# Kernel tuning notes

Hardware: AMD Instinct MI355X
Metric: run time of the kernel (lower is better)

## Reference

```python
import jax, jax.numpy as jnp
import numpy as np

NUM_ENT, NUM_REL, ES = 100000, 200, 128
B, N, K = 4, 1024, 50  # batch of tasks, triples per task, max one-hop neighbors


def setup_inputs() -> dict:
    key = jax.random.key(0)
    ks = jax.random.split(key, 10)
    return {
        "ent_emb": jax.random.normal(ks[0], (NUM_ENT, ES), jnp.float32),
        "rel_emb": jax.random.normal(ks[1], (NUM_REL, ES), jnp.float32),
        "W_bil": jax.random.normal(ks[2], (ES, ES), jnp.float32) * 0.05,
        "W1": jax.random.normal(ks[3], (ES, ES), jnp.float32) * 0.05,
        "b1": jax.random.normal(ks[4], (ES,), jnp.float32) * 0.05,
        "W2": jax.random.normal(ks[5], (ES, ES), jnp.float32) * 0.05,
        "b2": jax.random.normal(ks[6], (ES,), jnp.float32) * 0.05,
        "head_idx": jax.random.randint(ks[7], (B, N), 0, NUM_ENT, jnp.int64),
        "tail_idx": jax.random.randint(ks[8], (B, N), 0, NUM_ENT, jnp.int64),
        "conn_rel": jax.random.randint(ks[9], (NUM_ENT, K), 0, NUM_REL, jnp.int64),
    }


def reference(ent_emb, rel_emb, W_bil, W1, b1, W2, b2, head_idx, tail_idx, conn_rel):
    # Gather head/tail entity embeddings: [B, N, es]
    h_e = ent_emb[head_idx]
    t_e = ent_emb[tail_idx]
    weak_rel = t_e - h_e  # weak relation signal, [B, N, es]

    # Gather one-hop relation embeddings of head/tail neighborhoods: [B, N, K, es]
    h_rel = rel_emb[conn_rel[head_idx]]
    t_rel = rel_emb[conn_rel[tail_idx]]

    # Bilinear score (out_features=1, no bias): score = x1 @ W @ x2
    ws = jnp.einsum('ij,bnj->bni', W_bil, weak_rel)       # [B, N, es]
    h_att = jax.nn.softmax(jnp.einsum('bnki,bni->bnk', h_rel, ws), axis=-1)
    t_att = jax.nn.softmax(jnp.einsum('bnki,bni->bnk', t_rel, ws), axis=-1)

    # Attention-weighted aggregate over neighbors: [B, N, es]
    head = jnp.einsum('bnk,bnki->bni', h_att, h_rel)
    tail = jnp.einsum('bnk,bnki->bni', t_att, t_rel)

    # Fused linear + relu (torch Linear: x @ W.T + b)
    h = jax.nn.relu(head @ W1.T + b1 + h_e @ W2.T + b2)
    t = jax.nn.relu(tail @ W1.T + b1 + t_e @ W2.T + b2)

    # cat along the singleton dim=2 -> [B, N, 2, es]
    return jnp.stack((h, t), axis=2)
```

## Files before the change

kernel.cpp:

```cpp
#include <hip/hip_runtime.h>

#define ES 128
#define KN 50

__device__ __forceinline__ unsigned short f32_to_bf16_rne(float f) {
    unsigned u = __float_as_uint(f);
    unsigned r = u + 0x7FFF + ((u >> 16) & 1);
    return (unsigned short)(r >> 16);
}
__device__ __forceinline__ float bf16_to_f32(unsigned short u) {
    return __uint_as_float(((unsigned)u) << 16);
}

__global__ __launch_bounds__(128) void prep_rwb(
    const float* __restrict__ rel, const float* __restrict__ Wb,
    float* __restrict__ rwb)
{
    const int r = blockIdx.x, j = threadIdx.x;
    float acc = 0.f;
    #pragma unroll 8
    for (int i = 0; i < ES; ++i)
        acc += rel[r * ES + i] * Wb[i * ES + j];
    rwb[r * ES + j] = acc;
}

__global__ __launch_bounds__(256) void prep_wtbf(
    const float* __restrict__ W1, const float* __restrict__ W2,
    unsigned short* __restrict__ wtb)
{
    int n = blockIdx.x * 256 + threadIdx.x;
    int j = n >> 7, c = n & 127;
    const float* src = (j < ES) ? W1 : W2;
    wtb[n] = f32_to_bf16_rne(src[c * ES + (j & 127)]);
}

#define LOADC(BUF, C) do {                                                   \
    _Pragma("unroll") for (int u = 0; u < 5; ++u) {                          \
        int row = __shfl(cid, hb + 5 * (C) + u);                             \
        BUF[u] = *(const float4*)(RWb + (size_t)row * ES + 4 * q);           \
    } } while (0)

#define REDUCE(BUF, C) do {                                                  \
    float pv[5];                                                             \
    _Pragma("unroll") for (int u = 0; u < 5; ++u)                            \
        pv[u] = BUF[u].x*wr.x + BUF[u].y*wr.y + BUF[u].z*wr.z + BUF[u].w*wr.w;\
    _Pragma("unroll") for (int s = 1; s < 32; s <<= 1)                       \
        { _Pragma("unroll") for (int u = 0; u < 5; ++u)                      \
            pv[u] += __shfl_xor(pv[u], s); }                                 \
    _Pragma("unroll") for (int u = 0; u < 5; ++u)                            \
        s1 = (q == 5 * (C) + u) ? pv[u] : s1;                                \
    } while (0)

#define XADD(a) do { a.x += __shfl_xor(a.x, 32); a.y += __shfl_xor(a.y, 32); \
                     a.z += __shfl_xor(a.z, 32); a.w += __shfl_xor(a.w, 32); } while (0)

__global__ __launch_bounds__(256, 4) void onehop_main(
    const float* __restrict__ ent, const float* __restrict__ rel,
    const float* __restrict__ b1, const float* __restrict__ b2,
    const int* __restrict__ hidx, const int* __restrict__ tidx,
    const int* __restrict__ conn,
    const float* __restrict__ RWb, const unsigned short* __restrict__ WTB,
    float* __restrict__ out, int npair, int num_ent, int num_rel)
{
    __shared__ float coef[4][2 * ES];
    __shared__ float part[4][4][ES];

    const int tid  = threadIdx.x;
    const int w    = tid >> 6;
    const int lane = tid & 63;
    const int q    = lane & 31;
    const int hi   = lane >> 5;
    const int hb   = lane & 32;

    const int pair = min(blockIdx.x * 2 + (w >> 1), npair - 1);
    const int side = w & 1;

    int hid = min(max(hidx[pair], 0), num_ent - 1);
    int tdi = min(max(tidx[pair], 0), num_ent - 1);
    int eid = side ? tdi : hid;

    float4 he = *(const float4*)(ent + (size_t)hid * ES + 4 * q);
    float4 te = *(const float4*)(ent + (size_t)tdi * ES + 4 * q);
    float4 wr;
    wr.x = te.x - he.x; wr.y = te.y - he.y;
    wr.z = te.z - he.z; wr.w = te.w - he.w;
    if (!hi) *(float4*)(&coef[w][ES + 4 * q]) = side ? te : he;

    const int kl  = 25 * hi + min(q, 24);
    int cid = min(max(conn[(size_t)eid * KN + kl], 0), num_rel - 1);

    float s1 = -1e30f;
    {
        float4 buf[5];
        LOADC(buf, 0); REDUCE(buf, 0);
        LOADC(buf, 1); REDUCE(buf, 1);
        LOADC(buf, 2); REDUCE(buf, 2);
        LOADC(buf, 3); REDUCE(buf, 3);
        LOADC(buf, 4); REDUCE(buf, 4);
    }

    float m = s1;
    #pragma unroll
    for (int s = 1; s < 64; s <<= 1) m = fmaxf(m, __shfl_xor(m, s));
    float e1 = __expf(s1 - m);
    float l = e1;
    #pragma unroll
    for (int s = 1; s < 64; s <<= 1) l += __shfl_xor(l, s);
    e1 *= (1.f / l);

    float4 agg = {0.f, 0.f, 0.f, 0.f};
    #pragma unroll 5
    for (int t = 0; t < 25; ++t) {
        int src  = hb + t;
        float ev = __shfl(e1, src);
        int row  = __shfl(cid, src);
        float4 v = *(const float4*)(rel + (size_t)row * ES + 4 * q);
        agg.x += ev * v.x; agg.y += ev * v.y;
        agg.z += ev * v.z; agg.w += ev * v.w;
    }
    XADD(agg);
    if (!hi) *(float4*)(&coef[w][4 * q]) = agg;
    __syncthreads();

    const int jbase = w << 6;
    float4 a0 = {0,0,0,0}, a1 = {0,0,0,0}, a2 = {0,0,0,0}, a3 = {0,0,0,0};
    #pragma unroll 8
    for (int jj = 0; jj < 32; ++jj) {
        int j0 = jbase + 2 * jj;
        ushort4 wv = *(const ushort4*)(WTB + (size_t)j0 * ES + 4 * lane);
        float w0 = bf16_to_f32(wv.x), w1 = bf16_to_f32(wv.y);
        float w2 = bf16_to_f32(wv.z), w3 = bf16_to_f32(wv.w);
        int jl = j0 + hi;
        float c0 = coef[0][jl], c1 = coef[1][jl];
        float c2 = coef[2][jl], c3 = coef[3][jl];
        a0.x += c0*w0; a0.y += c0*w1; a0.z += c0*w2; a0.w += c0*w3;
        a1.x += c1*w0; a1.y += c1*w1; a1.z += c1*w2; a1.w += c1*w3;
        a2.x += c2*w0; a2.y += c2*w1; a2.z += c2*w2; a2.w += c2*w3;
        a3.x += c3*w0; a3.y += c3*w1; a3.z += c3*w2; a3.w += c3*w3;
    }
    XADD(a0); XADD(a1); XADD(a2); XADD(a3);
    if (!hi) {
        *(float4*)(&part[w][0][4 * q]) = a0;
        *(float4*)(&part[w][1][4 * q]) = a1;
        *(float4*)(&part[w][2][4 * q]) = a2;
        *(float4*)(&part[w][3][4 * q]) = a3;
    }
    __syncthreads();

    const int o = tid >> 6, c2i = tid & 63;
    float px = part[0][o][2*c2i]     + part[1][o][2*c2i]
             + part[2][o][2*c2i]     + part[3][o][2*c2i];
    float py = part[0][o][2*c2i + 1] + part[1][o][2*c2i + 1]
             + part[2][o][2*c2i + 1] + part[3][o][2*c2i + 1];
    float bx = b1[2*c2i]     + b2[2*c2i];
    float by = b1[2*c2i + 1] + b2[2*c2i + 1];
    const int opair = blockIdx.x * 2 + (o >> 1);
    if (opair < npair) {
        float2 r;
        r.x = fmaxf(px + bx, 0.f);
        r.y = fmaxf(py + by, 0.f);
        *(float2*)(out + (size_t)(opair * 2 + (o & 1)) * ES + 2 * c2i) = r;
    }
}

extern "C" void kernel_launch(void* const* d_in, const int* in_sizes, int n_in,
                              void* d_out, int out_size, void* d_ws, size_t ws_size,
                              hipStream_t stream) {
    const float* ent = (const float*)d_in[0];
    const float* rel = (const float*)d_in[1];
    const float* Wb  = (const float*)d_in[2];
    const float* W1  = (const float*)d_in[3];
    const float* b1  = (const float*)d_in[4];
    const float* W2  = (const float*)d_in[5];
    const float* b2  = (const float*)d_in[6];
    const int* hidx  = (const int*)d_in[7];
    const int* tidx  = (const int*)d_in[8];
    const int* conn  = (const int*)d_in[9];
    float* out = (float*)d_out;

    const int npair   = in_sizes[7];
    const int num_ent = in_sizes[0] / ES;
    const int num_rel = in_sizes[1] / ES;

    float* rwb = (float*)d_ws;
    unsigned short* wtb = (unsigned short*)(rwb + (size_t)num_rel * ES);

    prep_rwb<<<num_rel, 128, 0, stream>>>(rel, Wb, rwb);
    prep_wtbf<<<(2 * ES * ES) / 256, 256, 0, stream>>>(W1, W2, wtb);

    const int nblocks = (npair + 1) / 2;
    onehop_main<<<nblocks, 256, 0, stream>>>(
        ent, rel, b1, b2, hidx, tidx, conn,
        rwb, wtb, out, npair, num_ent, num_rel);
}
```

Baseline: 146.4 us.

## Split attention and output GEMM into separate kernels via bf16 intermediate

```diff
diff --git a/kernel.cpp b/kernel.cpp
--- a/kernel.cpp
+++ b/kernel.cpp
@@ -32,6 +32,13 @@
     int j = n >> 7, c = n & 127;
     const float* src = (j < ES) ? W1 : W2;
     wtb[n] = f32_to_bf16_rne(src[c * ES + (j & 127)]);
+}
+
+__global__ __launch_bounds__(256) void prep_relb(
+    const float* __restrict__ rel, unsigned short* __restrict__ relb, int n)
+{
+    int i = blockIdx.x * 256 + threadIdx.x;
+    if (i < n) relb[i] = f32_to_bf16_rne(rel[i]);
 }
 
 #define LOADC(BUF, C) do {                                                   \
@@ -54,17 +61,14 @@
 #define XADD(a) do { a.x += __shfl_xor(a.x, 32); a.y += __shfl_xor(a.y, 32); \
                      a.z += __shfl_xor(a.z, 32); a.w += __shfl_xor(a.w, 32); } while (0)
 
-__global__ __launch_bounds__(256, 4) void onehop_main(
-    const float* __restrict__ ent, const float* __restrict__ rel,
-    const float* __restrict__ b1, const float* __restrict__ b2,
+__global__ __launch_bounds__(256, 4) void onehop_attn(
+    const float* __restrict__ ent,
     const int* __restrict__ hidx, const int* __restrict__ tidx,
     const int* __restrict__ conn,
-    const float* __restrict__ RWb, const unsigned short* __restrict__ WTB,
-    float* __restrict__ out, int npair, int num_ent, int num_rel)
-{
-    __shared__ float coef[4][2 * ES];
-    __shared__ float part[4][4][ES];
-
+    const float* __restrict__ RWb, const unsigned short* __restrict__ RELB,
+    unsigned short* __restrict__ C,
+    int npair, int num_ent, int num_rel)
+{
     const int tid  = threadIdx.x;
     const int w    = tid >> 6;
     const int lane = tid & 63;
@@ -72,8 +76,9 @@
     const int hi   = lane >> 5;
     const int hb   = lane & 32;
 
-    const int pair = min(blockIdx.x * 2 + (w >> 1), npair - 1);
-    const int side = w & 1;
+    const int gw   = blockIdx.x * 4 + w;
+    const int pair = min(gw >> 1, npair - 1);
+    const int side = gw & 1;
 
     int hid = min(max(hidx[pair], 0), num_ent - 1);
     int tdi = min(max(tidx[pair], 0), num_ent - 1);
@@ -84,9 +89,8 @@
     float4 wr;
     wr.x = te.x - he.x; wr.y = te.y - he.y;
     wr.z = te.z - he.z; wr.w = te.w - he.w;
-    if (!hi) *(float4*)(&coef[w][ES + 4 * q]) = side ? te : he;
-
-    const int kl  = 25 * hi + min(q, 24);
+
+    const int kl = 25 * hi + min(q, 24);
     int cid = min(max(conn[(size_t)eid * KN + kl], 0), num_rel - 1);
 
     float s1 = -1e30f;
@@ -114,52 +118,86 @@
         int src  = hb + t;
         float ev = __shfl(e1, src);
         int row  = __shfl(cid, src);
-        float4 v = *(const float4*)(rel + (size_t)row * ES + 4 * q);
-        agg.x += ev * v.x; agg.y += ev * v.y;
-        agg.z += ev * v.z; agg.w += ev * v.w;
+        ushort4 v = *(const ushort4*)(RELB + (size_t)row * ES + 4 * q);
+        agg.x += ev * bf16_to_f32(v.x); agg.y += ev * bf16_to_f32(v.y);
+        agg.z += ev * bf16_to_f32(v.z); agg.w += ev * bf16_to_f32(v.w);
     }
     XADD(agg);
-    if (!hi) *(float4*)(&coef[w][4 * q]) = agg;
+
+    const int orow = pair * 2 + side;
+    float4 sv = hi ? (side ? te : he) : agg;
+    ushort4 o;
+    o.x = f32_to_bf16_rne(sv.x); o.y = f32_to_bf16_rne(sv.y);
+    o.z = f32_to_bf16_rne(sv.z); o.w = f32_to_bf16_rne(sv.w);
+    *(ushort4*)(C + (size_t)orow * 256 + (hi ? 128 : 0) + 4 * q) = o;
+}
+
+__global__ __launch_bounds__(256, 4) void gemm_out(
+    const unsigned short* __restrict__ C,
+    const unsigned short* __restrict__ WTB,
+    const float* __restrict__ b1, const float* __restrict__ b2,
+    float* __restrict__ out, int nrows)
+{
+    __shared__ unsigned int Cs[16 * 130];
+    const int tid  = threadIdx.x;
+    const int r    = tid >> 4;
+    const int cg   = tid & 15;
+    const int row0 = blockIdx.x * 16;
+
+    const unsigned int* Cg = (const unsigned int*)(C + (size_t)row0 * 256);
+    #pragma unroll
+    for (int i = 0; i < 8; ++i) {
+        int li = i * 256 + tid;
+        unsigned int v = (row0 + (li >> 7) < nrows) ? Cg[li] : 0u;
+        Cs[(li >> 7) * 130 + (li & 127)] = v;
+    }
     __syncthreads();
 
-    const int jbase = w << 6;
-    float4 a0 = {0,0,0,0}, a1 = {0,0,0,0}, a2 = {0,0,0,0}, a3 = {0,0,0,0};
-    #pragma unroll 8
-    for (int jj = 0; jj < 32; ++jj) {
-        int j0 = jbase + 2 * jj;
-        ushort4 wv = *(const ushort4*)(WTB + (size_t)j0 * ES + 4 * lane);
-        float w0 = bf16_to_f32(wv.x), w1 = bf16_to_f32(wv.y);
-        float w2 = bf16_to_f32(wv.z), w3 = bf16_to_f32(wv.w);
-        int jl = j0 + hi;
-        float c0 = coef[0][jl], c1 = coef[1][jl];
-        float c2 = coef[2][jl], c3 = coef[3][jl];
-        a0.x += c0*w0; a0.y += c0*w1; a0.z += c0*w2; a0.w += c0*w3;
-        a1.x += c1*w0; a1.y += c1*w1; a1.z += c1*w2; a1.w += c1*w3;
-        a2.x += c2*w0; a2.y += c2*w1; a2.z += c2*w2; a2.w += c2*w3;
-        a3.x += c3*w0; a3.y += c3*w1; a3.z += c3*w2; a3.w += c3*w3;
-    }
-    XADD(a0); XADD(a1); XADD(a2); XADD(a3);
-    if (!hi) {
-        *(float4*)(&part[w][0][4 * q]) = a0;
-        *(float4*)(&part[w][1][4 * q]) = a1;
-        *(float4*)(&part[w][2][4 * q]) = a2;
-        *(float4*)(&part[w][3][4 * q]) = a3;
-    }
-    __syncthreads();
-
-    const int o = tid >> 6, c2i = tid & 63;
-    float px = part[0][o][2*c2i]     + part[1][o][2*c2i]
-             + part[2][o][2*c2i]     + part[3][o][2*c2i];
-    float py = part[0][o][2*c2i + 1] + part[1][o][2*c2i + 1]
-             + part[2][o][2*c2i + 1] + part[3][o][2*c2i + 1];
-    float bx = b1[2*c2i]     + b2[2*c2i];
-    float by = b1[2*c2i + 1] + b2[2*c2i + 1];
-    const int opair = blockIdx.x * 2 + (o >> 1);
-    if (opair < npair) {
-        float2 r;
-        r.x = fmaxf(px + bx, 0.f);
-        r.y = fmaxf(py + by, 0.f);
-        *(float2*)(out + (size_t)(opair * 2 + (o & 1)) * ES + 2 * c2i) = r;
+    float acc[8] = {0,0,0,0,0,0,0,0};
+    const unsigned int* Wg = (const unsigned int*)WTB;
+    #pragma unroll 4
+    for (int k2 = 0; k2 < 128; ++k2) {
+        unsigned int cd = Cs[r * 130 + k2];
+        float c0 = __uint_as_float(cd << 16);
+        float c1 = __uint_as_float(cd & 0xffff0000u);
+        uint4 w0 = *(const uint4*)(Wg + (size_t)(2 * k2)     * 64 + cg * 4);
+        uint4 w1 = *(const uint4*)(Wg + (size_t)(2 * k2 + 1) * 64 + cg * 4);
+        acc[0] += c0 * __uint_as_float(w0.x << 16);
+        acc[1] += c0 * __uint_as_float(w0.x & 0xffff0000u);
+        acc[2] += c0 * __uint_as_float(w0.y << 16);
+        acc[3] += c0 * __uint_as_float(w0.y & 0xffff0000u);
+        acc[4] += c0 * __uint_as_float(w0.z << 16);
+        acc[5] += c0 * __uint_as_float(w0.z & 0xffff0000u);
+        acc[6] += c0 * __uint_as_float(w0.w << 16);
+        acc[7] += c0 * __uint_as_float(w0.w & 0xffff0000u);
+        acc[0] += c1 * __uint_as_float(w1.x << 16);
+        acc[1] += c1 * __uint_as_float(w1.x & 0xffff0000u);
+        acc[2] += c1 * __uint_as_float(w1.y << 16);
+        acc[3] += c1 * __uint_as_float(w1.y & 0xffff0000u);
+        acc[4] += c1 * __uint_as_float(w1.z << 16);
+        acc[5] += c1 * __uint_as_float(w1.z & 0xffff0000u);
+        acc[6] += c1 * __uint_as_float(w1.w << 16);
+        acc[7] += c1 * __uint_as_float(w1.w & 0xffff0000u);
+    }
+
+    const int col0 = cg * 8;
+    float4 p1a = *(const float4*)(b1 + col0);
+    float4 p1b = *(const float4*)(b1 + col0 + 4);
+    float4 p2a = *(const float4*)(b2 + col0);
+    float4 p2b = *(const float4*)(b2 + col0 + 4);
+    float4 o0, o1;
+    o0.x = fmaxf(acc[0] + p1a.x + p2a.x, 0.f);
+    o0.y = fmaxf(acc[1] + p1a.y + p2a.y, 0.f);
+    o0.z = fmaxf(acc[2] + p1a.z + p2a.z, 0.f);
+    o0.w = fmaxf(acc[3] + p1a.w + p2a.w, 0.f);
+    o1.x = fmaxf(acc[4] + p1b.x + p2b.x, 0.f);
+    o1.y = fmaxf(acc[5] + p1b.y + p2b.y, 0.f);
+    o1.z = fmaxf(acc[6] + p1b.z + p2b.z, 0.f);
+    o1.w = fmaxf(acc[7] + p1b.w + p2b.w, 0.f);
+    const int row = row0 + r;
+    if (row < nrows) {
+        *(float4*)(out + (size_t)row * ES + col0)     = o0;
+        *(float4*)(out + (size_t)row * ES + col0 + 4) = o1;
     }
 }
 
@@ -181,15 +219,20 @@
     const int npair   = in_sizes[7];
     const int num_ent = in_sizes[0] / ES;
     const int num_rel = in_sizes[1] / ES;
+    const int nrows   = 2 * npair;
 
     float* rwb = (float*)d_ws;
-    unsigned short* wtb = (unsigned short*)(rwb + (size_t)num_rel * ES);
+    unsigned short* wtb  = (unsigned short*)(rwb + (size_t)num_rel * ES);
+    unsigned short* relb = wtb + 2 * ES * ES;
+    unsigned short* Cm   = relb + (size_t)num_rel * ES;
 
     prep_rwb<<<num_rel, 128, 0, stream>>>(rel, Wb, rwb);
     prep_wtbf<<<(2 * ES * ES) / 256, 256, 0, stream>>>(W1, W2, wtb);
-
-    const int nblocks = (npair + 1) / 2;
-    onehop_main<<<nblocks, 256, 0, stream>>>(
-        ent, rel, b1, b2, hidx, tidx, conn,
-        rwb, wtb, out, npair, num_ent, num_rel);
-}
+    prep_relb<<<(num_rel * ES + 255) / 256, 256, 0, stream>>>(rel, relb, num_rel * ES);
+
+    onehop_attn<<<(nrows + 3) / 4, 256, 0, stream>>>(
+        ent, hidx, tidx, conn, rwb, relb, Cm, npair, num_ent, num_rel);
+
+    gemm_out<<<(nrows + 15) / 16, 256, 0, stream>>>(
+        Cm, wtb, b1, b2, out, nrows);
+}
```

Result: slower. 157.4 us (+7.5%).
